# Performance work log

Hardware: AMD Instinct MI355X
Metric: run time of the kernel (lower is better)

The kernel has to match this reference:

```python
import jax, jax.numpy as jnp
import numpy as np

K = 4
TEMP = 34.0
KS = 3
PAD = 1
STRIDE = 1


def setup_inputs() -> dict:
    key = jax.random.key(0)
    k0, k1, k2, k3, k4, k5 = jax.random.split(key, 6)
    B, C, H, W = 32, 256, 56, 56
    OC = 256
    HID = int(C * 0.25) + 1  # 65
    x = jax.random.normal(k0, (B, C, H, W), jnp.float32)
    # kaiming-ish scales for the 1x1 attention convs (treated as matmuls)
    w_fc1 = jax.random.normal(k1, (HID, C), jnp.float32) * np.float32(np.sqrt(2.0 / C))
    w_fc2 = jax.random.normal(k2, (K, HID), jnp.float32) * np.float32(np.sqrt(2.0 / HID))
    b_fc2 = jnp.zeros((K,), jnp.float32)
    # positive step sizes for numerical sanity (torch inits randn then overwrites at init_state)
    alpha = jax.random.uniform(k3, (K, 1), jnp.float32, minval=0.05, maxval=1.0)
    weight = jax.random.normal(k4, (K, OC, C, KS, KS), jnp.float32) * 0.05
    bias_w = jax.random.normal(k5, (K, OC), jnp.float32) * 0.01
    return dict(x=x, w_fc1=w_fc1, w_fc2=w_fc2, b_fc2=b_fc2, alpha=alpha,
                weight=weight, bias_w=bias_w)


def _round_ste(v):
    # round_pass: forward round, backward identity
    return v + jax.lax.stop_gradient(jnp.round(v) - v)


def _lsq_quant(w2d, alpha):
    # Faithful to the torch LSQQuantizer forward (eval path): divide by per-row
    # alpha, clamp ONLY scalar elements [0,0],[1,0],[2,0] (as the torch code does),
    # then straight-through round and rescale. grad_scale copies into .data and
    # therefore has no effect on values or the autograd graph.
    d = w2d / alpha  # (K, M)
    d = d.at[0, 0].set(jnp.clip(d[0, 0], -2.0, 1.0))   # 2-bit range
    d = d.at[1, 0].set(jnp.clip(d[1, 0], -4.0, 3.0))   # 3-bit range
    d = d.at[2, 0].set(jnp.clip(d[2, 0], -8.0, 7.0))   # 4-bit range
    return _round_ste(d) * alpha


def reference(x, w_fc1, w_fc2, b_fc2, alpha, weight, bias_w):
    B, C, H, W = x.shape
    Kk, OC = bias_w.shape
    # attention2d: global avg pool -> 1x1 conv -> relu -> 1x1 conv (+bias)
    pooled = x.mean(axis=(2, 3))                     # (B, C)
    h = jax.nn.relu(pooled @ w_fc1.T)                # (B, HID)
    raw = h @ w_fc2.T + b_fc2                        # (B, K)
    # gradient_approximation: forward = one-hot(argmax), backward = softmax(x/T)
    soft = jax.nn.softmax(raw / TEMP, axis=1)
    hard = jax.nn.one_hot(jnp.argmax(raw, axis=1), Kk, dtype=raw.dtype)
    attn = soft + jax.lax.stop_gradient(hard - soft)  # (B, K)
    # LSQ-quantize flattened expert weights, then per-sample aggregation
    wq = _lsq_quant(weight.reshape(Kk, -1), alpha)   # (K, OC*C*KS*KS)
    agg_w = (attn @ wq).reshape(B, OC, C, KS, KS)    # per-sample kernels
    agg_b = attn @ bias_w                            # (B, OC)
    # per-sample conv2d (equivalent to the groups=batch trick)
    def conv1(xb, wb):
        return jax.lax.conv_general_dilated(
            xb[None], wb, (STRIDE, STRIDE), [(PAD, PAD), (PAD, PAD)],
            dimension_numbers=('NCHW', 'OIHW', 'NCHW'))[0]
    out = jax.vmap(conv1)(x, agg_w) + agg_b[:, :, None, None]  # (B, OC, H, W)
    return (out, raw)
```

## Files before the change

### kernel.cpp

```cpp
#include <hip/hip_runtime.h>
#include <hip/hip_bf16.h>

typedef __attribute__((ext_vector_type(8))) short short8;
typedef __attribute__((ext_vector_type(16))) float f32x16;

#define XPAD_OFF   0u
#define WQ_OFF     55115776u
#define POOL_OFF   59834368u
#define IDX_OFF    59867136u

__device__ __forceinline__ void gl_lds16(const void* g, void* l) {
  __builtin_amdgcn_global_load_lds(
      (const __attribute__((address_space(1))) unsigned int*)g,
      (__attribute__((address_space(3))) unsigned int*)l, 16, 0, 0);
}

__global__ __launch_bounds__(128) void fc_argmax_kernel(
    const float* __restrict__ pooled, const float* __restrict__ w_fc1,
    const float* __restrict__ w_fc2, const float* __restrict__ b_fc2,
    float* __restrict__ raw_out, int* __restrict__ idx) {
  __shared__ float h[65];
  __shared__ float raws[4];
  const int b = blockIdx.x, t = threadIdx.x;
  if (t < 65) {
    float s = 0.f;
    const float4* pb = (const float4*)(pooled + b * 256);
    const float4* wr = (const float4*)(w_fc1 + t * 256);
    for (int c = 0; c < 64; ++c) {
      const float4 a4 = pb[c], b4 = wr[c];
      s += a4.x * b4.x + a4.y * b4.y + a4.z * b4.z + a4.w * b4.w;
    }
    s *= (1.0f / 3136.0f);
    h[t] = s > 0.f ? s : 0.f;
  }
  __syncthreads();
  if (t < 4) {
    float s = b_fc2[t];
    const float* wr = w_fc2 + t * 65;
    for (int j = 0; j < 65; ++j) s += h[j] * wr[j];
    raws[t] = s;
    raw_out[b * 4 + t] = s;
  }
  __syncthreads();
  if (t == 0) {
    int best = 0; float bv = raws[0];
    for (int k = 1; k < 4; ++k) if (raws[k] > bv) { bv = raws[k]; best = k; }
    idx[b] = best;
  }
}

__global__ __launch_bounds__(256) void quant_kernel(
    const float* __restrict__ weight, const float* __restrict__ alpha,
    __hip_bfloat16* __restrict__ Wq, float* __restrict__ pooled) {
  __shared__ __attribute__((aligned(16))) float Ws[32 * 292];
  const int tid = threadIdx.x;
  const int B = blockIdx.x;
  if (B == 0) {
    for (int i = tid; i < 8192; i += 256) pooled[i] = 0.f;
  }
  const int cbh    = B & 7;
  const int octile = (B >> 3) & 1;
  const int wm     = (B >> 4) & 1;
  const int ot     = (B >> 5) & 1;
  const int k      = B >> 6;
  const int oc0 = ot * 128 + wm * 64 + octile * 32;

  const int ocr = tid >> 3, q = tid & 7;
  const float4* src = (const float4*)weight +
                      (size_t)k * 147456 + (size_t)(oc0 + ocr) * 576 + cbh * 72;
  #pragma unroll
  for (int j = 0; j < 9; ++j) {
    const float4 v = src[q + 8 * j];
    *(float4*)&Ws[ocr * 292 + 4 * (q + 8 * j)] = v;
  }
  __syncthreads();

  const int p    = tid >> 7;
  const int s    = (tid >> 6) & 1;
  const int lane = tid & 63;
  const int ocl  = lane & 31;
  const int khl  = lane >> 5;
  const float a = alpha[k];
  const int ubase = ((k * 2 + ot) * 9) * 64 + (cbh * 8 + wm * 4 + octile * 2 + s);
  #pragma unroll
  for (int m = 0; m < 5; ++m) {
    const int tap = 2 * m + p;
    if (tap > 8) break;
    union { short8 v; __hip_bfloat16 e[8]; } uo;
    #pragma unroll
    for (int cl = 0; cl < 8; ++cl) {
      const int chl = s * 16 + khl * 8 + cl;
      float v = Ws[ocl * 292 + chl * 9 + tap] / a;
      if (oc0 == 0 && ocl == 0 && cbh == 0 && chl == 0 && tap == 0) {
        if (k == 0)      v = fminf(fmaxf(v, -2.f), 1.f);
        else if (k == 1) v = fminf(fmaxf(v, -4.f), 3.f);
        else if (k == 2) v = fminf(fmaxf(v, -8.f), 7.f);
      }
      uo.e[cl] = __float2bfloat16(rintf(v) * a);
    }
    const size_t u = (size_t)(ubase + tap * 64);
    *(short8*)&Wq[u * 512 + lane * 8] = uo.v;
  }
}

__global__ __launch_bounds__(512) void padx_kernel(const float* __restrict__ x,
                                                   __hip_bfloat16* __restrict__ Xpad,
                                                   float* __restrict__ pooled) {
  __shared__ __attribute__((aligned(16))) __hip_bfloat16 T2[2][56][264];
  const int q = blockIdx.x;
  const int b = blockIdx.y;
  const int tid = threadIdx.x;
  const int r = tid >> 8;
  const int c = tid & 255;
  const int yp  = 2 * q + r;
  const int yin = yp - 1;
  if (yin >= 0 && yin < 56) {
    const float4* src = (const float4*)(x + ((size_t)(b * 256 + c) * 3136 + yin * 56));
    float4 v[14];
    #pragma unroll
    for (int i = 0; i < 14; ++i) v[i] = src[i];
    float s = 0.f;
    #pragma unroll
    for (int i = 0; i < 14; ++i) {
      s += v[i].x + v[i].y + v[i].z + v[i].w;
      T2[r][4 * i + 0][c] = __float2bfloat16(v[i].x);
      T2[r][4 * i + 1][c] = __float2bfloat16(v[i].y);
      T2[r][4 * i + 2][c] = __float2bfloat16(v[i].z);
      T2[r][4 * i + 3][c] = __float2bfloat16(v[i].w);
    }
    atomicAdd(pooled + b * 256 + c, s);
  }
  __syncthreads();
  const short8 zero8 = (short8){0, 0, 0, 0, 0, 0, 0, 0};
  for (int i = tid; i < 3712; i += 512) {
    const int cg  = i & 31;
    const int px  = (i >> 5) % 58;
    const int rr  = i / (58 * 32);
    const int ypo = 2 * q + rr;
    const int yio = ypo - 1;
    short8 v;
    if (yio < 0 || yio >= 56 || px == 0 || px == 57) v = zero8;
    else v = *(const short8*)&T2[rr][px - 1][cg * 8];
    *(short8*)(Xpad + (((size_t)(b * 58 + ypo) * 58 + px) * 256 + cg * 8)) = v;
  }
}

__global__ __launch_bounds__(256, 2) void conv_kernel(
    const __hip_bfloat16* __restrict__ Xpad, const __hip_bfloat16* __restrict__ Wq,
    const int* __restrict__ idx, const float* __restrict__ bias_w,
    float* __restrict__ out) {
  __shared__ __attribute__((aligned(16))) __hip_bfloat16 Xs[22784];

  const int tid = threadIdx.x;
  const int lane = tid & 63;
  const int w = tid >> 6;
  const int wm = w & 1;
  const int wn = w >> 1;

  const int b  = blockIdx.x;
  const int pt = blockIdx.y >> 1;
  const int ot = blockIdx.y & 1;
  const int Y0 = pt * 4;
  const int OC0 = ot * 128;
  const int kb = idx[b];

  const __hip_bfloat16* xb = Xpad + (size_t)b * (58 * 58 * 256);
  const short8* W0 = (const short8*)Wq + (size_t)(kb * 2 + ot) * 36864;

  f32x16 acc[2][4];
  #pragma unroll
  for (int i = 0; i < 2; ++i)
    #pragma unroll
    for (int j = 0; j < 4; ++j)
      acc[i][j] = (f32x16){0,0,0,0,0,0,0,0,0,0,0,0,0,0,0,0};

  const int nlo = lane & 31;
  const int khalf = lane >> 5;

  auto stageseg = [&](int cbn, int bufsel, int k) {
    int sidx = k * 64 + lane;
    int p = sidx >> 2;
    if (p > 347) p = 347;
    const int gsel = (sidx & 3) ^ ((p >> 1) & 3);
    const int r = p / 58, xc = p - r * 58;
    gl_lds16(xb + (((Y0 + r) * 58 + xc) * 256 + cbn * 32 + gsel * 8),
             (char*)Xs + bufsel * 22784 + k * 1024);
  };

  for (int k = w; k < 22; k += 4) stageseg(0, 0, k);
  __syncthreads();

  short8 afr[3][4];
  #pragma unroll
  for (int oc2 = 0; oc2 < 2; ++oc2)
    #pragma unroll
    for (int s2 = 0; s2 < 2; ++s2) {
      afr[0][oc2 * 2 + s2] = W0[0 * 4096 + 0 * 512 + wm * 256 + oc2 * 128 + s2 * 64 + lane];
      afr[1][oc2 * 2 + s2] = W0[1 * 4096 + 0 * 512 + wm * 256 + oc2 * 128 + s2 * 64 + lane];
    }

  for (int cbh = 0; cbh < 8; ++cbh) {
    const __hip_bfloat16* cur = Xs + (cbh & 1) * 11392;
    const int nb = (cbh + 1) & 1;

    #pragma unroll
    for (int t = 0; t < 9; ++t) {
      const int dy = t / 3, dx = t - dy * 3;
      if (cbh < 7) {
        if (t < 5) stageseg(cbh + 1, nb, w + 4 * t);
        else if (t == 5 && w < 2) stageseg(cbh + 1, nb, w + 20);
      }
      if (cbh < 7 || t < 7) {
        const int tap2 = (t + 2) % 9, cb2 = cbh + (t + 2) / 9;
        #pragma unroll
        for (int oc2 = 0; oc2 < 2; ++oc2)
          #pragma unroll
          for (int s2 = 0; s2 < 2; ++s2)
            afr[(t + 2) % 3][oc2 * 2 + s2] =
                W0[tap2 * 4096 + cb2 * 512 + wm * 256 + oc2 * 128 + s2 * 64 + lane];
      }
      #pragma unroll
      for (int s = 0; s < 2; ++s) {
        #pragma unroll
        for (int j = 0; j < 4; ++j) {
          const int row = wn * 2 + (j >> 1) + dy;
          const int col = (j & 1) * 32 + nlo + dx;
          const int p = row * 58 + col;
          const int slot = p * 4 + ((s * 2 + khalf) ^ ((p >> 1) & 3));
          const short8 bfr = *(const short8*)&cur[slot * 8];
          #pragma unroll
          for (int i = 0; i < 2; ++i)
            acc[i][j] = __builtin_amdgcn_mfma_f32_32x32x16_bf16(
                afr[t % 3][i * 2 + s], bfr, acc[i][j], 0, 0, 0);
        }
      }
    }
    __syncthreads();
  }

  const float* biasb = bias_w + kb * 256;
  #pragma unroll
  for (int i = 0; i < 2; ++i) {
    #pragma unroll
    for (int j = 0; j < 4; ++j) {
      const int xcol = (j & 1) * 32 + nlo;
      if (xcol < 56) {
        const int y = Y0 + wn * 2 + (j >> 1);
        #pragma unroll
        for (int reg = 0; reg < 16; ++reg) {
          const int row = (reg & 3) + 8 * (reg >> 2) + 4 * khalf;
          const int oc = OC0 + wm * 64 + i * 32 + row;
          out[(((size_t)b * 256 + oc) * 56 + y) * 56 + xcol] =
              acc[i][j][reg] + biasb[oc];
        }
      }
    }
  }
}

extern "C" void kernel_launch(void* const* d_in, const int* in_sizes, int n_in,
                              void* d_out, int out_size, void* d_ws, size_t ws_size,
                              hipStream_t stream) {
  const float* x      = (const float*)d_in[0];
  const float* w_fc1  = (const float*)d_in[1];
  const float* w_fc2  = (const float*)d_in[2];
  const float* b_fc2  = (const float*)d_in[3];
  const float* alpha  = (const float*)d_in[4];
  const float* weight = (const float*)d_in[5];
  const float* bias_w = (const float*)d_in[6];

  float* out = (float*)d_out;
  float* raw_out = out + (size_t)32 * 256 * 56 * 56;

  char* ws = (char*)d_ws;
  __hip_bfloat16* Xpad = (__hip_bfloat16*)(ws + XPAD_OFF);
  __hip_bfloat16* Wq   = (__hip_bfloat16*)(ws + WQ_OFF);
  float* pooled        = (float*)(ws + POOL_OFF);
  int* idx             = (int*)(ws + IDX_OFF);

  quant_kernel<<<256, 256, 0, stream>>>(weight, alpha, Wq, pooled);
  padx_kernel<<<dim3(29, 32), 512, 0, stream>>>(x, Xpad, pooled);
  fc_argmax_kernel<<<32, 128, 0, stream>>>(pooled, w_fc1, w_fc2, b_fc2, raw_out, idx);
  conv_kernel<<<dim3(32, 28), 256, 0, stream>>>(Xpad, Wq, idx, bias_w, out);
}
```

Before: 333.8 us.

## Give each wave all 128 output channels and one image row, double-buffer weights

Changes the per-wave tile from 64 output channels × 2 rows to 128 output channels × 1 row, so each wave issues four A fragments per B fragment. This halves the LDS reads of activation fragments per MFMA but doubles the weight fragments each wave holds and loads from global memory. The weight prefetch buffer shrinks from three stages to two, with a lookahead of one tap instead of two. The channel-block loop is unrolled by two with compile-time parity so the buffer indices are constant. The trade-offs are higher VGPR pressure, which risks occupancy at launch_bounds(256,2), and less latency hiding for the weight loads.

```diff
diff --git a/kernel.cpp b/kernel.cpp
--- a/kernel.cpp
+++ b/kernel.cpp
@@ -1,5 +1,6 @@
 #include <hip/hip_runtime.h>
 #include <hip/hip_bf16.h>
+#include <type_traits>
 
 typedef __attribute__((ext_vector_type(8))) short short8;
 typedef __attribute__((ext_vector_type(16))) float f32x16;
@@ -154,8 +155,6 @@
   const int tid = threadIdx.x;
   const int lane = tid & 63;
   const int w = tid >> 6;
-  const int wm = w & 1;
-  const int wn = w >> 1;
 
   const int b  = blockIdx.x;
   const int pt = blockIdx.y >> 1;
@@ -167,11 +166,11 @@
   const __hip_bfloat16* xb = Xpad + (size_t)b * (58 * 58 * 256);
   const short8* W0 = (const short8*)Wq + (size_t)(kb * 2 + ot) * 36864;
 
-  f32x16 acc[2][4];
-  #pragma unroll
-  for (int i = 0; i < 2; ++i)
-    #pragma unroll
-    for (int j = 0; j < 4; ++j)
+  f32x16 acc[4][2];
+  #pragma unroll
+  for (int i = 0; i < 4; ++i)
+    #pragma unroll
+    for (int j = 0; j < 2; ++j)
       acc[i][j] = (f32x16){0,0,0,0,0,0,0,0,0,0,0,0,0,0,0,0};
 
   const int nlo = lane & 31;
@@ -190,19 +189,18 @@
   for (int k = w; k < 22; k += 4) stageseg(0, 0, k);
   __syncthreads();
 
-  short8 afr[3][4];
-  #pragma unroll
-  for (int oc2 = 0; oc2 < 2; ++oc2)
-    #pragma unroll
-    for (int s2 = 0; s2 < 2; ++s2) {
-      afr[0][oc2 * 2 + s2] = W0[0 * 4096 + 0 * 512 + wm * 256 + oc2 * 128 + s2 * 64 + lane];
-      afr[1][oc2 * 2 + s2] = W0[1 * 4096 + 0 * 512 + wm * 256 + oc2 * 128 + s2 * 64 + lane];
-    }
-
-  for (int cbh = 0; cbh < 8; ++cbh) {
-    const __hip_bfloat16* cur = Xs + (cbh & 1) * 11392;
-    const int nb = (cbh + 1) & 1;
-
+  short8 afr[2][8];
+  #pragma unroll
+  for (int i2 = 0; i2 < 4; ++i2)
+    #pragma unroll
+    for (int s2 = 0; s2 < 2; ++s2)
+      afr[0][i2 * 2 + s2] =
+          W0[(i2 >> 1) * 256 + (i2 & 1) * 128 + s2 * 64 + lane];
+
+  auto chunk = [&](int cbh, auto parc) {
+    constexpr int PAR = decltype(parc)::value;
+    const __hip_bfloat16* cur = Xs + PAR * 11392;
+    const int nb = PAR ^ 1;
     #pragma unroll
     for (int t = 0; t < 9; ++t) {
       const int dy = t / 3, dx = t - dy * 3;
@@ -210,46 +208,52 @@
         if (t < 5) stageseg(cbh + 1, nb, w + 4 * t);
         else if (t == 5 && w < 2) stageseg(cbh + 1, nb, w + 20);
       }
-      if (cbh < 7 || t < 7) {
-        const int tap2 = (t + 2) % 9, cb2 = cbh + (t + 2) / 9;
+      if (cbh < 7 || t < 8) {
+        const int tap2 = (t + 1) % 9, cb2 = cbh + (t + 1) / 9;
         #pragma unroll
-        for (int oc2 = 0; oc2 < 2; ++oc2)
+        for (int i2 = 0; i2 < 4; ++i2)
           #pragma unroll
           for (int s2 = 0; s2 < 2; ++s2)
-            afr[(t + 2) % 3][oc2 * 2 + s2] =
-                W0[tap2 * 4096 + cb2 * 512 + wm * 256 + oc2 * 128 + s2 * 64 + lane];
+            afr[(t + 1 + PAR) & 1][i2 * 2 + s2] =
+                W0[tap2 * 4096 + cb2 * 512 + (i2 >> 1) * 256 + (i2 & 1) * 128 +
+                   s2 * 64 + lane];
       }
       #pragma unroll
       for (int s = 0; s < 2; ++s) {
         #pragma unroll
-        for (int j = 0; j < 4; ++j) {
-          const int row = wn * 2 + (j >> 1) + dy;
-          const int col = (j & 1) * 32 + nlo + dx;
+        for (int j = 0; j < 2; ++j) {
+          const int row = w + dy;
+          const int col = j * 32 + nlo + dx;
           const int p = row * 58 + col;
           const int slot = p * 4 + ((s * 2 + khalf) ^ ((p >> 1) & 3));
           const short8 bfr = *(const short8*)&cur[slot * 8];
           #pragma unroll
-          for (int i = 0; i < 2; ++i)
+          for (int i = 0; i < 4; ++i)
             acc[i][j] = __builtin_amdgcn_mfma_f32_32x32x16_bf16(
-                afr[t % 3][i * 2 + s], bfr, acc[i][j], 0, 0, 0);
+                afr[(t + PAR) & 1][i * 2 + s], bfr, acc[i][j], 0, 0, 0);
         }
       }
     }
     __syncthreads();
+  };
+
+  for (int c2 = 0; c2 < 8; c2 += 2) {
+    chunk(c2,     std::integral_constant<int, 0>{});
+    chunk(c2 + 1, std::integral_constant<int, 1>{});
   }
 
   const float* biasb = bias_w + kb * 256;
-  #pragma unroll
-  for (int i = 0; i < 2; ++i) {
-    #pragma unroll
-    for (int j = 0; j < 4; ++j) {
-      const int xcol = (j & 1) * 32 + nlo;
-      if (xcol < 56) {
-        const int y = Y0 + wn * 2 + (j >> 1);
+  const int y = Y0 + w;
+  #pragma unroll
+  for (int j = 0; j < 2; ++j) {
+    const int xcol = j * 32 + nlo;
+    if (xcol < 56) {
+      #pragma unroll
+      for (int i = 0; i < 4; ++i) {
         #pragma unroll
         for (int reg = 0; reg < 16; ++reg) {
-          const int row = (reg & 3) + 8 * (reg >> 2) + 4 * khalf;
-          const int oc = OC0 + wm * 64 + i * 32 + row;
+          const int rowr = (reg & 3) + 8 * (reg >> 2) + 4 * khalf;
+          const int oc = OC0 + (i >> 1) * 64 + (i & 1) * 32 + rowr;
           out[(((size_t)b * 256 + oc) * 56 + y) * 56 + xcol] =
               acc[i][j][reg] + biasb[oc];
         }
```

New measurement: 380.5 us. 1.14x slower.
